# Kernel optimization log

Hardware: AMD Instinct MI355X
Metric: run time of the kernel (lower is better)

The kernel has to match this reference:

```python
import jax, jax.numpy as jnp
import numpy as np


def setup_inputs() -> dict:
    key = jax.random.key(0)
    k1, k2, k3 = jax.random.split(key, 3)
    B, Cout, Cin, H, W = 8, 64, 64, 256, 256
    Wf_rfft = W // 2 + 1
    init_scale = 0.1
    x = jax.random.normal(k1, (B, Cout, H, W), dtype=jnp.float32)
    weight_fft = jax.random.normal(k2, (Cout, Cin, H, Wf_rfft), dtype=jnp.float32) * init_scale
    bias = jax.random.normal(k3, (Cin,), dtype=jnp.float32) * init_scale
    return {"x": x, "weight_fft": weight_fft, "bias": bias}


def reference(x, weight_fft, bias):
    # x: (B, Cout, H, W); weight_fft: (Cout, Cin, Hf, Wf_rfft); bias: (Cin,)
    B, Cout, H, W = x.shape
    _, Cin, Hf, Wf_rfft = weight_fft.shape
    X_fft = jnp.fft.rfft2(x, axes=(2, 3))  # (B, Cout, H, W//2+1) complex
    # Channel contraction over Cout per frequency bin (original code does a
    # broadcast multiply-then-sum; einsum computes identical math without
    # materializing the (B,Cout,Cin,Hf,Wf) intermediate).
    Z_fft = jnp.einsum('bohw,oihw->bihw', X_fft, weight_fft.astype(X_fft.dtype))
    real_Wf = 2 * (Wf_rfft - 1) if Wf_rfft > 1 else 1
    y = jnp.fft.irfft2(Z_fft, s=(Hf, real_Wf), axes=(2, 3))
    y = y[..., :H, :W]
    return y + bias[None, :, None, None]
```

## Files before the change

kernel.cpp:

```cpp
#include <hip/hip_runtime.h>
#include <hip/hip_bf16.h>
#include <math.h>

#define PI_F 3.14159265358979323846f


__device__ __forceinline__ unsigned pack_bf(float re, float im) {
    unsigned ur = __float_as_uint(re);
    unsigned ui = __float_as_uint(im);
    ur = (ur + 0x7fffu + ((ur >> 16) & 1u)) >> 16;
    ui = (ui + 0x7fffu + ((ui >> 16) & 1u)) & 0xffff0000u;
    return ur | ui;
}
__device__ __forceinline__ float2 unpack_bf(unsigned p) {
    return make_float2(__uint_as_float(p << 16),
                       __uint_as_float(p & 0xffff0000u));
}

__device__ __forceinline__ int s2i(int p) { return p ^ (((p >> 4) & 3) << 2); }

__device__ __forceinline__ float2 cadd(float2 a, float2 b){ return make_float2(a.x+b.x, a.y+b.y); }
__device__ __forceinline__ float2 csub(float2 a, float2 b){ return make_float2(a.x-b.x, a.y-b.y); }
__device__ __forceinline__ float2 cmul(float2 a, float2 b){ return make_float2(a.x*b.x-a.y*b.y, a.x*b.y+a.y*b.x); }

template<int SGN>
__device__ __forceinline__ void quad2(float2& u0, float2& u1, float2& u2, float2& u3,
                                      int jt, float invh) {
    const float th = (SGN < 0 ? -PI_F : PI_F) * (float)jt * invh;
    float s2v, c2;
    __sincosf(0.5f * th, &s2v, &c2);
    const float c1 = c2 * c2 - s2v * s2v;
    const float s1 = 2.0f * c2 * s2v;
    const float2 w1 = make_float2(c1, s1), w2 = make_float2(c2, s2v);
    const float2 t1 = cmul(w1, u1), t3 = cmul(w1, u3);
    const float2 v0 = cadd(u0, t1), v1 = csub(u0, t1);
    const float2 v2 = cadd(u2, t3), v3 = csub(u2, t3);
    const float2 t2 = cmul(w2, v2);
    float2 t4 = cmul(w2, v3);
    t4 = (SGN < 0) ? make_float2(t4.y, -t4.x) : make_float2(-t4.y, t4.x);
    u0 = cadd(v0, t2); u2 = csub(v0, t2);
    u1 = cadd(v1, t4); u3 = csub(v1, t4);
}

template<int SGN>
__device__ __forceinline__ void fft256(float2* w, int j,
                                       float2& o0, float2& o1, float2& o2, float2& o3) {
    const int r = (int)(__brev((unsigned)j) >> 26);
    float2 u0 = w[s2i(r)], u1 = w[s2i(r + 128)], u2 = w[s2i(r + 64)], u3 = w[s2i(r + 192)];
    __builtin_amdgcn_wave_barrier();
    {
        const float2 v0 = cadd(u0, u1), v1 = csub(u0, u1);
        const float2 v2 = cadd(u2, u3), v3 = csub(u2, u3);
        const float2 t4 = (SGN < 0) ? make_float2(v3.y, -v3.x) : make_float2(-v3.y, v3.x);
        u0 = cadd(v0, v2); u2 = csub(v0, v2);
        u1 = cadd(v1, t4); u3 = csub(v1, t4);
    }
    const int p4 = s2i(4 * j);
    *(float4*)&w[p4]     = make_float4(u0.x, u0.y, u1.x, u1.y);
    *(float4*)&w[p4 + 2] = make_float4(u2.x, u2.y, u3.x, u3.y);
    __builtin_amdgcn_wave_barrier();
    {
        const int jt = j & 3;
        const int p = ((j >> 2) << 4) | jt;
        float2 a0 = w[s2i(p)], a1 = w[s2i(p+4)], a2 = w[s2i(p+8)], a3 = w[s2i(p+12)];
        quad2<SGN>(a0, a1, a2, a3, jt, 0.25f);
        w[s2i(p)] = a0; w[s2i(p+4)] = a1; w[s2i(p+8)] = a2; w[s2i(p+12)] = a3;
    }
    __builtin_amdgcn_wave_barrier();
    {
        const int jt = j & 15;
        const int p = ((j >> 4) << 6) | jt;
        float2 a0 = w[s2i(p)], a1 = w[s2i(p+16)], a2 = w[s2i(p+32)], a3 = w[s2i(p+48)];
        quad2<SGN>(a0, a1, a2, a3, jt, 1.0f/16.0f);
        w[s2i(p)] = a0; w[s2i(p+16)] = a1; w[s2i(p+32)] = a2; w[s2i(p+48)] = a3;
    }
    __builtin_amdgcn_wave_barrier();
    {
        float2 a0 = w[s2i(j)], a1 = w[s2i(j+64)], a2 = w[s2i(j+128)], a3 = w[s2i(j+192)];
        quad2<SGN>(a0, a1, a2, a3, j, 1.0f/64.0f);
        o0 = a0; o1 = a1; o2 = a2; o3 = a3;
    }
}

#define SMEM_BYTES (132096 + 8 * 256 * 8)

__global__ __launch_bounds__(512) void k_fwd2d(const float* __restrict__ x,
                                               unsigned* __restrict__ Xf) {
    extern __shared__ char smem[];
    unsigned* S = (unsigned*)smem;
    float2* w = (float2*)(smem + 132096) + ((threadIdx.x >> 6) << 8);
    const int t = threadIdx.x, f = t >> 6, j = t & 63;
    const int bo = blockIdx.x;
    const float* xi = x + (size_t)bo * 65536;

    for (int r = f; r < 256; r += 8) {
        const float4 v = ((const float4*)(xi + (r << 8)))[j];
        const int p4 = s2i(4 * j);
        *(float4*)&w[p4]     = make_float4(v.x, 0.0f, v.y, 0.0f);
        *(float4*)&w[p4 + 2] = make_float4(v.z, 0.0f, v.w, 0.0f);
        __builtin_amdgcn_wave_barrier();
        float2 o0, o1, o2, o3;
        fft256<-1>(w, j, o0, o1, o2, o3);
        S[r * 129 + j]      = pack_bf(o0.x, o0.y);
        S[r * 129 + 64 + j] = pack_bf(o1.x, o1.y);
        if (j == 0) S[r * 129 + 128] = pack_bf(o2.x, o2.y);
        __builtin_amdgcn_wave_barrier();
    }
    __syncthreads();
    for (int c = f; c <= 128; c += 8) {
#pragma unroll
        for (int k = 0; k < 4; ++k)
            w[s2i(j + 64 * k)] = unpack_bf(S[(j + 64 * k) * 129 + c]);
        __builtin_amdgcn_wave_barrier();
        float2 o0, o1, o2, o3;
        fft256<-1>(w, j, o0, o1, o2, o3);
        S[(j      ) * 129 + c] = pack_bf(o0.x, o0.y);
        S[(j +  64) * 129 + c] = pack_bf(o1.x, o1.y);
        S[(j + 128) * 129 + c] = pack_bf(o2.x, o2.y);
        S[(j + 192) * 129 + c] = pack_bf(o3.x, o3.y);
        __builtin_amdgcn_wave_barrier();
    }
    __syncthreads();
    uint4* dst = (uint4*)(Xf + (size_t)bo * 33024);
    const uint4* src4 = (const uint4*)S;
    for (int e = t; e < 8256; e += 512) dst[e] = src4[e];
}

__global__ __launch_bounds__(256) void k_einsum(unsigned* __restrict__ Xf,
                                                const float* __restrict__ Wt) {
    __shared__ unsigned xs[512][32];
    const int t = threadIdx.x;
    const int bid = blockIdx.x;
    const int nid = (bid & 7) * 129 + (bid >> 3);
    const size_t n0 = (size_t)nid * 32;

#pragma unroll
    for (int k = 0; k < 16; ++k) {
        const int e = t + 256 * k;
        const int pr = e >> 3, q = e & 7;
        const uint4 v = *reinterpret_cast<const uint4*>(
            Xf + (size_t)pr * 33024 + n0 + (q << 2));
        *reinterpret_cast<uint4*>(&xs[pr][q << 2]) = v;
    }
    __syncthreads();

    const int nl = t & 31, j = t >> 5;
    float2 acc[8][8];
#pragma unroll
    for (int r = 0; r < 8; ++r)
#pragma unroll
        for (int b = 0; b < 8; ++b) acc[r][b] = make_float2(0.0f, 0.0f);

    const float* Wb = Wt + n0 + nl;
    auto wload = [&](int o, float (&buf)[8]) {
#pragma unroll
        for (int r = 0; r < 8; ++r)
            buf[r] = __builtin_nontemporal_load(
                Wb + (size_t)((o << 6) | ((r << 3) | j)) * 33024);
    };
    auto fmab = [&](int o, const float (&wc)[8]) {
        float2 xv[8];
#pragma unroll
        for (int b = 0; b < 8; ++b) xv[b] = unpack_bf(xs[(b << 6) | o][nl]);
#pragma unroll
        for (int r = 0; r < 8; ++r)
#pragma unroll
            for (int b = 0; b < 8; ++b) {
                acc[r][b].x += xv[b].x * wc[r];
                acc[r][b].y += xv[b].y * wc[r];
            }
    };

    float wA[8], wB[8];
    wload(0, wA);
    wload(1, wB);
    for (int o = 0; o < 64; o += 2) {
        float wc0[8];
#pragma unroll
        for (int r = 0; r < 8; ++r) wc0[r] = wA[r];
        wload((o + 2) & 63, wA);
        fmab(o, wc0);
        float wc1[8];
#pragma unroll
        for (int r = 0; r < 8; ++r) wc1[r] = wB[r];
        wload((o + 3) & 63, wB);
        fmab(o + 1, wc1);
    }

#pragma unroll
    for (int r = 0; r < 8; ++r) {
        const int i = (r << 3) | j;
#pragma unroll
        for (int b = 0; b < 8; ++b) {
            Xf[(size_t)((b << 6) | i) * 33024 + n0 + nl] =
                pack_bf(acc[r][b].x, acc[r][b].y);
        }
    }
}

__global__ __launch_bounds__(512) void k_inv2d(const unsigned* __restrict__ Xf,
                                               const float* __restrict__ bias,
                                               float* __restrict__ y) {
    extern __shared__ char smem[];
    unsigned* S = (unsigned*)smem;
    float2* w = (float2*)(smem + 132096) + ((threadIdx.x >> 6) << 8);
    const int t = threadIdx.x, f = t >> 6, j = t & 63;
    const int bo = blockIdx.x;
    const float bv = bias[bo & 63];

    {
        uint4* s4 = (uint4*)S;
        const uint4* g4 = (const uint4*)(Xf + (size_t)bo * 33024);
        for (int e = t; e < 8256; e += 512) s4[e] = g4[e];
    }
    __syncthreads();
    for (int c = f; c <= 128; c += 8) {
#pragma unroll
        for (int k = 0; k < 4; ++k)
            w[s2i(j + 64 * k)] = unpack_bf(S[(j + 64 * k) * 129 + c]);
        __builtin_amdgcn_wave_barrier();
        float2 o0, o1, o2, o3;
        fft256<+1>(w, j, o0, o1, o2, o3);
        S[(j      ) * 129 + c] = pack_bf(o0.x, o0.y);
        S[(j +  64) * 129 + c] = pack_bf(o1.x, o1.y);
        S[(j + 128) * 129 + c] = pack_bf(o2.x, o2.y);
        S[(j + 192) * 129 + c] = pack_bf(o3.x, o3.y);
        __builtin_amdgcn_wave_barrier();
    }
    __syncthreads();
    float* yo = y + (size_t)bo * 65536;
    for (int r = f; r < 256; r += 8) {
        const unsigned* Sr = S + r * 129;
        float2 a0 = unpack_bf(Sr[j]);
        float2 a1 = unpack_bf(Sr[j + 64]);
        float2 a2;
        if (j == 0) a2 = unpack_bf(Sr[128]);
        else { a2 = unpack_bf(Sr[128 - j]); a2.y = -a2.y; }
        float2 a3 = unpack_bf(Sr[64 - j]); a3.y = -a3.y;
        w[s2i(j)]       = a0;
        w[s2i(j +  64)] = a1;
        w[s2i(j + 128)] = a2;
        w[s2i(j + 192)] = a3;
        __builtin_amdgcn_wave_barrier();
        float2 o0, o1, o2, o3;
        fft256<+1>(w, j, o0, o1, o2, o3);
        const float sc = 1.0f / 65536.0f;
        float* yr = yo + (r << 8);
        __builtin_nontemporal_store(o0.x * sc + bv, yr + j);
        __builtin_nontemporal_store(o1.x * sc + bv, yr + j + 64);
        __builtin_nontemporal_store(o2.x * sc + bv, yr + j + 128);
        __builtin_nontemporal_store(o3.x * sc + bv, yr + j + 192);
        __builtin_amdgcn_wave_barrier();
    }
}

extern "C" void kernel_launch(void* const* d_in, const int* in_sizes, int n_in,
                              void* d_out, int out_size, void* d_ws,
                              size_t ws_size, hipStream_t stream) {
    (void)in_sizes; (void)n_in; (void)out_size; (void)ws_size;
    const float* x    = (const float*)d_in[0];
    const float* wfft = (const float*)d_in[1];
    const float* bias = (const float*)d_in[2];
    float* y = (float*)d_out;
    unsigned* Xf = (unsigned*)d_ws;

    hipFuncSetAttribute((const void*)k_fwd2d,
                        hipFuncAttributeMaxDynamicSharedMemorySize, SMEM_BYTES);
    hipFuncSetAttribute((const void*)k_inv2d,
                        hipFuncAttributeMaxDynamicSharedMemorySize, SMEM_BYTES);

    k_fwd2d<<<512, 512, SMEM_BYTES, stream>>>(x, Xf);
    k_einsum<<<1032, 256, 0, stream>>>(Xf, wfft);
    k_inv2d<<<512, 512, SMEM_BYTES, stream>>>(Xf, bias, y);
}
```

Before: 333.4 us.

## Pack two real rows per complex FFT in forward and inverse row passes

Uses the two-for-one real FFT trick: two real rows are packed as real and imaginary parts of one complex 256-point FFT. In the forward pass the two spectra are separated with a lane shuffle and conjugate-symmetry arithmetic. In the inverse pass two Hermitian spectra are combined so that one complex inverse FFT yields both real output rows. This halves the number of row FFTs in both kernels, at the cost of extra shuffles and separation arithmetic, plus some extra bf16 rounding exposure from the combined values.

Result: faster. 286.6 us (-14.0%).

```diff
diff --git a/kernel.cpp b/kernel.cpp
--- a/kernel.cpp
+++ b/kernel.cpp
@@ -93,17 +93,36 @@
     const int bo = blockIdx.x;
     const float* xi = x + (size_t)bo * 65536;
 
-    for (int r = f; r < 256; r += 8) {
-        const float4 v = ((const float4*)(xi + (r << 8)))[j];
+    for (int rp = f; rp < 128; rp += 8) {
+        const int r1 = rp, r2 = rp + 128;
+        const float4 va = ((const float4*)(xi + (r1 << 8)))[j];
+        const float4 vb = ((const float4*)(xi + (r2 << 8)))[j];
         const int p4 = s2i(4 * j);
-        *(float4*)&w[p4]     = make_float4(v.x, 0.0f, v.y, 0.0f);
-        *(float4*)&w[p4 + 2] = make_float4(v.z, 0.0f, v.w, 0.0f);
+        *(float4*)&w[p4]     = make_float4(va.x, vb.x, va.y, vb.y);
+        *(float4*)&w[p4 + 2] = make_float4(va.z, vb.z, va.w, vb.w);
         __builtin_amdgcn_wave_barrier();
         float2 o0, o1, o2, o3;
         fft256<-1>(w, j, o0, o1, o2, o3);
-        S[r * 129 + j]      = pack_bf(o0.x, o0.y);
-        S[r * 129 + 64 + j] = pack_bf(o1.x, o1.y);
-        if (j == 0) S[r * 129 + 128] = pack_bf(o2.x, o2.y);
+        const int src = (64 - j) & 63;
+        float2 P3, P2;
+        P3.x = __shfl(o3.x, src); P3.y = __shfl(o3.y, src);
+        P2.x = __shfl(o2.x, src); P2.y = __shfl(o2.y, src);
+        const float2 Cj = (j == 0) ? make_float2(o0.x, -o0.y)
+                                   : make_float2(P3.x, -P3.y);
+        const float2 Ck = (j == 0) ? make_float2(P3.x, -P3.y)
+                                   : make_float2(P2.x, -P2.y);
+        const float2 Aj = make_float2(0.5f * (o0.x + Cj.x), 0.5f * (o0.y + Cj.y));
+        const float2 Bj = make_float2(0.5f * (o0.y - Cj.y), -0.5f * (o0.x - Cj.x));
+        const float2 Ak = make_float2(0.5f * (o1.x + Ck.x), 0.5f * (o1.y + Ck.y));
+        const float2 Bk = make_float2(0.5f * (o1.y - Ck.y), -0.5f * (o1.x - Ck.x));
+        S[r1 * 129 + j]      = pack_bf(Aj.x, Aj.y);
+        S[r1 * 129 + 64 + j] = pack_bf(Ak.x, Ak.y);
+        S[r2 * 129 + j]      = pack_bf(Bj.x, Bj.y);
+        S[r2 * 129 + 64 + j] = pack_bf(Bk.x, Bk.y);
+        if (j == 0) {
+            S[r1 * 129 + 128] = pack_bf(o2.x, 0.0f);
+            S[r2 * 129 + 128] = pack_bf(o2.y, 0.0f);
+        }
         __builtin_amdgcn_wave_barrier();
     }
     __syncthreads();
@@ -229,27 +248,41 @@
     }
     __syncthreads();
     float* yo = y + (size_t)bo * 65536;
-    for (int r = f; r < 256; r += 8) {
-        const unsigned* Sr = S + r * 129;
-        float2 a0 = unpack_bf(Sr[j]);
-        float2 a1 = unpack_bf(Sr[j + 64]);
-        float2 a2;
-        if (j == 0) a2 = unpack_bf(Sr[128]);
-        else { a2 = unpack_bf(Sr[128 - j]); a2.y = -a2.y; }
-        float2 a3 = unpack_bf(Sr[64 - j]); a3.y = -a3.y;
-        w[s2i(j)]       = a0;
-        w[s2i(j +  64)] = a1;
-        w[s2i(j + 128)] = a2;
-        w[s2i(j + 192)] = a3;
+    for (int rp = f; rp < 128; rp += 8) {
+        const int r1 = rp, r2 = rp + 128;
+        const unsigned* Sa = S + r1 * 129;
+        const unsigned* Sb = S + r2 * 129;
+        const float2 A0 = unpack_bf(Sa[j]),      B0 = unpack_bf(Sb[j]);
+        const float2 A1 = unpack_bf(Sa[j + 64]), B1 = unpack_bf(Sb[j + 64]);
+        const int i2 = (j == 0) ? 128 : 128 - j;
+        const float2 A2 = unpack_bf(Sa[i2]),     B2 = unpack_bf(Sb[i2]);
+        const float2 A3 = unpack_bf(Sa[64 - j]), B3 = unpack_bf(Sb[64 - j]);
+        const float2 z0 = (j == 0)
+            ? make_float2(A0.x, B0.x)
+            : make_float2(A0.x - B0.y, A0.y + B0.x);
+        const float2 z1 = make_float2(A1.x - B1.y, A1.y + B1.x);
+        const float2 z2 = (j == 0)
+            ? make_float2(A2.x, B2.x)
+            : make_float2(A2.x + B2.y, B2.x - A2.y);
+        const float2 z3 = make_float2(A3.x + B3.y, B3.x - A3.y);
+        w[s2i(j)]       = z0;
+        w[s2i(j +  64)] = z1;
+        w[s2i(j + 128)] = z2;
+        w[s2i(j + 192)] = z3;
         __builtin_amdgcn_wave_barrier();
         float2 o0, o1, o2, o3;
         fft256<+1>(w, j, o0, o1, o2, o3);
         const float sc = 1.0f / 65536.0f;
-        float* yr = yo + (r << 8);
-        __builtin_nontemporal_store(o0.x * sc + bv, yr + j);
-        __builtin_nontemporal_store(o1.x * sc + bv, yr + j + 64);
-        __builtin_nontemporal_store(o2.x * sc + bv, yr + j + 128);
-        __builtin_nontemporal_store(o3.x * sc + bv, yr + j + 192);
+        float* y1 = yo + (r1 << 8);
+        float* y2 = yo + (r2 << 8);
+        __builtin_nontemporal_store(o0.x * sc + bv, y1 + j);
+        __builtin_nontemporal_store(o1.x * sc + bv, y1 + j + 64);
+        __builtin_nontemporal_store(o2.x * sc + bv, y1 + j + 128);
+        __builtin_nontemporal_store(o3.x * sc + bv, y1 + j + 192);
+        __builtin_nontemporal_store(o0.y * sc + bv, y2 + j);
+        __builtin_nontemporal_store(o1.y * sc + bv, y2 + j + 64);
+        __builtin_nontemporal_store(o2.y * sc + bv, y2 + j + 128);
+        __builtin_nontemporal_store(o3.y * sc + bv, y2 + j + 192);
         __builtin_amdgcn_wave_barrier();
     }
 }
```
